# Kernel tuning notes

Hardware: AMD Instinct MI355X
Metric: run time of the kernel (lower is better)

Reference implementation:

```python
import jax, jax.numpy as jnp
import numpy as np
import math

D = 512      # input_size == hidden_size
TAU = 4      # length of att/spatial lists
N = 16384    # tokens (batch*H*W)

def setup_inputs() -> dict:
    key = jax.random.key(0)
    ks = jax.random.split(key, 16)
    s = 1.0 / math.sqrt(D)
    return {
        "T_t": jax.random.normal(ks[0], (N, D), jnp.float32),
        "S_t": jax.random.normal(ks[1], (N, D), jnp.float32),
        "t_att": jax.random.normal(ks[2], (TAU, N, D), jnp.float32),
        "s_att": jax.random.normal(ks[3], (TAU, N, D), jnp.float32),
        "t_spatial": jax.random.normal(ks[4], (TAU, N, D), jnp.float32),
        "s_spatial": jax.random.normal(ks[5], (TAU, N, D), jnp.float32),
        # fl_t: Linear(D, 3D); fl_t_next: Linear(D, D); same for s
        "W_t": jax.random.uniform(ks[6], (3 * D, D), jnp.float32, -s, s),
        "b_t": jax.random.uniform(ks[7], (3 * D,), jnp.float32, -s, s),
        "W_tn": jax.random.uniform(ks[8], (D, D), jnp.float32, -s, s),
        "b_tn": jax.random.uniform(ks[9], (D,), jnp.float32, -s, s),
        "W_s": jax.random.uniform(ks[10], (3 * D, D), jnp.float32, -s, s),
        "b_s": jax.random.uniform(ks[11], (3 * D,), jnp.float32, -s, s),
        "W_sn": jax.random.uniform(ks[12], (D, D), jnp.float32, -s, s),
        "b_sn": jax.random.uniform(ks[13], (D,), jnp.float32, -s, s),
    }

def reference(T_t, S_t, t_att, s_att, t_spatial, s_spatial,
              W_t, b_t, W_tn, b_tn, W_s, b_s, W_sn, b_sn):
    d = T_t.shape[-1]
    scale = 1.0 / jnp.sqrt(jnp.asarray(d, T_t.dtype))
    s_next = S_t @ W_sn.T + b_sn          # [N, D]
    t_next = T_t @ W_tn.T + b_tn          # [N, D]

    # trend weights: dot-product along feature dim, softmax over tau axis
    w_s = jax.nn.softmax(jnp.einsum('knd,nd->kn', s_att, s_next) * scale, axis=0)
    w_t = jax.nn.softmax(jnp.einsum('knd,nd->kn', t_spatial, t_next) * scale, axis=0)
    T_trend = jnp.einsum('knd,kn->nd', t_att, w_s)      # [N, D]
    S_trend = jnp.einsum('knd,kn->nd', s_spatial, w_t)  # [N, D]

    t_gate = jax.nn.sigmoid(t_next)
    s_gate = jax.nn.sigmoid(s_next)
    T_fusion = T_t * t_gate + (1.0 - t_gate) * T_trend
    S_fusion = S_t * s_gate + (1.0 - s_gate) * S_trend

    T_concat = T_fusion @ W_t.T + b_t     # [N, 3D]
    S_concat = S_fusion @ W_s.T + b_s
    t_g, t_t, t_s = jnp.split(T_concat, 3, axis=1)
    s_g, s_t, s_s = jnp.split(S_concat, 3, axis=1)
    T_gate = jax.nn.sigmoid(t_g)
    S_gate = jax.nn.sigmoid(s_g)
    T_new = T_gate * t_t + (1.0 - T_gate) * s_t
    S_new = S_gate * s_s + (1.0 - S_gate) * t_s
    return T_new, S_new
```

## Files before the change

### kernel.cpp

```cpp
#include <hip/hip_runtime.h>

#define NTOK 16384
#define DIM 512
#define NTAU 4

typedef __attribute__((ext_vector_type(4))) float f32x4;
typedef __attribute__((ext_vector_type(8))) short bf16x8;
typedef __attribute__((ext_vector_type(4))) unsigned short u16x4;
typedef __attribute__((ext_vector_type(8))) unsigned short u16x8;
typedef unsigned int u32;

__device__ inline unsigned short f2bf(float f) {
    union { float f; unsigned int u; } v; v.f = f;
    unsigned int u = v.u + 0x7FFFu + ((v.u >> 16) & 1u);
    return (unsigned short)(u >> 16);
}

__device__ inline void bf8_to_f32(u16x8 h, f32x4& a, f32x4& b) {
    union { unsigned int u; float f; } t;
#pragma unroll
    for (int e = 0; e < 4; e++) { t.u = ((unsigned int)h[e]) << 16; a[e] = t.f; }
#pragma unroll
    for (int e = 0; e < 4; e++) { t.u = ((unsigned int)h[4 + e]) << 16; b[e] = t.f; }
}

#define NTLOAD4(p) __builtin_nontemporal_load((const f32x4*)(p))

__device__ __forceinline__ void gload16(const void* g, void* l) {
    __builtin_amdgcn_global_load_lds((const __attribute__((address_space(1))) u32*)g,
                                     (__attribute__((address_space(3))) u32*)l, 16, 0, 0);
}

__global__ void convert_all(const float* __restrict__ a, const float* __restrict__ b,
                            const float* __restrict__ c, const float* __restrict__ d,
                            unsigned short* __restrict__ oa, unsigned short* __restrict__ ob,
                            unsigned short* __restrict__ oc, unsigned short* __restrict__ od) {
    int i = blockIdx.x * 256 + threadIdx.x;
    const float* s; unsigned short* t; int off;
    if (i < 65536)       { s = a; t = oa; off = i; }
    else if (i < 131072) { s = b; t = ob; off = i - 65536; }
    else if (i < 327680) { s = c; t = oc; off = i - 131072; }
    else                 { s = d; t = od; off = i - 327680; }
    f32x4 v = ((const f32x4*)s)[off];
    u16x4 o;
    o[0] = f2bf(v[0]); o[1] = f2bf(v[1]); o[2] = f2bf(v[2]); o[3] = f2bf(v[3]);
    ((u16x4*)t)[off] = o;
}

__global__ __launch_bounds__(256, 2) void gemm_next2(
    const float* __restrict__ T_t, const float* __restrict__ S_t,
    const unsigned short* __restrict__ Wtn, const unsigned short* __restrict__ Wsn,
    const float* __restrict__ btn, const float* __restrict__ bsn,
    unsigned short* __restrict__ t_next, unsigned short* __restrict__ s_next)
{
    __shared__ unsigned short lA[128][40];
    __shared__ unsigned short lB[128][40];
    const int tid = threadIdx.x;
    const int id = blockIdx.x;
    const int xcd = id & 7;
    const int rest = id >> 3;
    const int mat = rest & 1;
    const int idx = rest >> 1;
    const float* A = mat ? S_t : T_t;
    const unsigned short* W = mat ? Wsn : Wtn;
    const float* bias = mat ? bsn : btn;
    unsigned short* out = mat ? s_next : t_next;
    const int m0 = (xcd * 16 + (idx >> 2)) * 128;
    const int n0 = (idx & 3) * 128;
    const int lane = tid & 63;
    const int w = tid >> 6;
    const int wr = w >> 1, wc = w & 1;

    f32x4 acc[4][4];
#pragma unroll
    for (int i = 0; i < 4; i++)
#pragma unroll
        for (int j = 0; j < 4; j++) acc[i][j] = (f32x4){0.f, 0.f, 0.f, 0.f};

    const int arow = tid >> 3;
    const int acol = (tid & 7) * 4;
    const int brow = tid >> 2;
    const int bcol = (tid & 3) * 8;

    for (int k0 = 0; k0 < DIM; k0 += 32) {
#pragma unroll
        for (int i = 0; i < 4; i++) {
            int r = arow + 32 * i;
            f32x4 v = *(const f32x4*)(A + (size_t)(m0 + r) * DIM + k0 + acol);
            u16x4 o;
            o[0] = f2bf(v[0]); o[1] = f2bf(v[1]); o[2] = f2bf(v[2]); o[3] = f2bf(v[3]);
            *(u16x4*)&lA[r][acol] = o;
        }
#pragma unroll
        for (int i = 0; i < 2; i++) {
            int r = brow + 64 * i;
            u16x8 v = *(const u16x8*)(W + (size_t)(n0 + r) * DIM + k0 + bcol);
            *(u16x8*)&lB[r][bcol] = v;
        }
        __syncthreads();

        bf16x8 af[4], bfr[4];
#pragma unroll
        for (int i = 0; i < 4; i++)
            af[i] = *(const bf16x8*)&lA[wr * 64 + i * 16 + (lane & 15)][(lane >> 4) * 8];
#pragma unroll
        for (int j = 0; j < 4; j++)
            bfr[j] = *(const bf16x8*)&lB[wc * 64 + j * 16 + (lane & 15)][(lane >> 4) * 8];
#pragma unroll
        for (int i = 0; i < 4; i++)
#pragma unroll
            for (int j = 0; j < 4; j++)
                acc[i][j] = __builtin_amdgcn_mfma_f32_16x16x32_bf16(af[i], bfr[j], acc[i][j], 0, 0, 0);
        __syncthreads();
    }

#pragma unroll
    for (int j = 0; j < 4; j++) {
        int n = n0 + wc * 64 + j * 16 + (lane & 15);
        float bv = bias[n];
#pragma unroll
        for (int i = 0; i < 4; i++) {
            int mbase = m0 + wr * 64 + i * 16 + (lane >> 4) * 4;
#pragma unroll
            for (int r = 0; r < 4; r++)
                out[(size_t)(mbase + r) * DIM + n] = f2bf(acc[i][j][r] + bv);
        }
    }
}

__global__ __launch_bounds__(256) void dots_kernel(
    const float* __restrict__ s_att, const float* __restrict__ t_spatial,
    const unsigned short* __restrict__ t_next, const unsigned short* __restrict__ s_next,
    float* __restrict__ w_all)
{
    const int lane = threadIdx.x & 63;
    const int id = blockIdx.x;
    const int n = (id & 7) * 2048 + (id >> 3) * 4 + (threadIdx.x >> 6);
    const int c = lane * 8;
    const size_t rb = (size_t)n * DIM + c;
    const float scale = 0.04419417382415922f;

    f32x4 tn_a, tn_b, sn_a, sn_b;
    bf8_to_f32(*(const u16x8*)(t_next + rb), tn_a, tn_b);
    bf8_to_f32(*(const u16x8*)(s_next + rb), sn_a, sn_b);

    float dws[NTAU], dwt[NTAU];
#pragma unroll
    for (int k = 0; k < NTAU; k++) {
        const size_t kb = ((size_t)k * NTOK + n) * DIM + c;
        f32x4 a0 = NTLOAD4(s_att + kb);
        f32x4 a1 = NTLOAD4(s_att + kb + 4);
        f32x4 b0 = NTLOAD4(t_spatial + kb);
        f32x4 b1 = NTLOAD4(t_spatial + kb + 4);
        dws[k] = a0[0]*sn_a[0]+a0[1]*sn_a[1]+a0[2]*sn_a[2]+a0[3]*sn_a[3]
               + a1[0]*sn_b[0]+a1[1]*sn_b[1]+a1[2]*sn_b[2]+a1[3]*sn_b[3];
        dwt[k] = b0[0]*tn_a[0]+b0[1]*tn_a[1]+b0[2]*tn_a[2]+b0[3]*tn_a[3]
               + b1[0]*tn_b[0]+b1[1]*tn_b[1]+b1[2]*tn_b[2]+b1[3]*tn_b[3];
    }
#pragma unroll
    for (int k = 0; k < NTAU; k++) {
        float v = dws[k];
#pragma unroll
        for (int off = 32; off; off >>= 1) v += __shfl_xor(v, off);
        dws[k] = v * scale;
        float u = dwt[k];
#pragma unroll
        for (int off = 32; off; off >>= 1) u += __shfl_xor(u, off);
        dwt[k] = u * scale;
    }

    float ms = fmaxf(fmaxf(dws[0], dws[1]), fmaxf(dws[2], dws[3]));
    float mt = fmaxf(fmaxf(dwt[0], dwt[1]), fmaxf(dwt[2], dwt[3]));
    f32x4 wsv, wtv;
    float ssum = 0.f, tsum = 0.f;
#pragma unroll
    for (int k = 0; k < NTAU; k++) {
        wsv[k] = __expf(dws[k] - ms); ssum += wsv[k];
        wtv[k] = __expf(dwt[k] - mt); tsum += wtv[k];
    }
    float rs = 1.f / ssum, rt = 1.f / tsum;
#pragma unroll
    for (int k = 0; k < NTAU; k++) { wsv[k] *= rs; wtv[k] *= rt; }

    if (lane == 0) {
        *(f32x4*)(w_all + (size_t)n * 8)     = wsv;
        *(f32x4*)(w_all + (size_t)n * 8 + 4) = wtv;
    }
}

__global__ __launch_bounds__(256) void fusion_kernel(
    const float* __restrict__ T_t, const float* __restrict__ S_t,
    const float* __restrict__ t_att, const float* __restrict__ s_spatial,
    const unsigned short* __restrict__ t_next, const unsigned short* __restrict__ s_next,
    const float* __restrict__ w_all,
    unsigned short* __restrict__ Tf, unsigned short* __restrict__ Sf)
{
    const int lane = threadIdx.x & 63;
    const int id = blockIdx.x;
    const int n = (id & 7) * 2048 + (id >> 3) * 4 + (threadIdx.x >> 6);
    const int c = lane * 8;
    const size_t rb = (size_t)n * DIM + c;

    f32x4 wsv = *(const f32x4*)(w_all + (size_t)n * 8);
    f32x4 wtv = *(const f32x4*)(w_all + (size_t)n * 8 + 4);

    f32x4 Tta = {0,0,0,0}, Ttb = {0,0,0,0}, Sta = {0,0,0,0}, Stb = {0,0,0,0};
#pragma unroll
    for (int k = 0; k < NTAU; k++) {
        const size_t kb = ((size_t)k * NTOK + n) * DIM + c;
        f32x4 ta = NTLOAD4(t_att + kb);
        f32x4 tb = NTLOAD4(t_att + kb + 4);
        f32x4 sa = NTLOAD4(s_spatial + kb);
        f32x4 sb = NTLOAD4(s_spatial + kb + 4);
        float wk = wsv[k], vk = wtv[k];
#pragma unroll
        for (int e = 0; e < 4; e++) {
            Tta[e] += wk * ta[e]; Ttb[e] += wk * tb[e];
            Sta[e] += vk * sa[e]; Stb[e] += vk * sb[e];
        }
    }

    f32x4 tn_a, tn_b, sn_a, sn_b;
    bf8_to_f32(*(const u16x8*)(t_next + rb), tn_a, tn_b);
    bf8_to_f32(*(const u16x8*)(s_next + rb), sn_a, sn_b);
    f32x4 Ta = NTLOAD4(T_t + rb);
    f32x4 Tb = NTLOAD4(T_t + rb + 4);
    f32x4 Sa = NTLOAD4(S_t + rb);
    f32x4 Sb = NTLOAD4(S_t + rb + 4);

    u16x8 oT, oS;
#pragma unroll
    for (int e = 0; e < 4; e++) {
        float gt_a = 1.f / (1.f + __expf(-tn_a[e]));
        float gt_b = 1.f / (1.f + __expf(-tn_b[e]));
        float gs_a = 1.f / (1.f + __expf(-sn_a[e]));
        float gs_b = 1.f / (1.f + __expf(-sn_b[e]));
        oT[e]     = f2bf(Ta[e] * gt_a + (1.f - gt_a) * Tta[e]);
        oT[4 + e] = f2bf(Tb[e] * gt_b + (1.f - gt_b) * Ttb[e]);
        oS[e]     = f2bf(Sa[e] * gs_a + (1.f - gs_a) * Sta[e]);
        oS[4 + e] = f2bf(Sb[e] * gs_b + (1.f - gs_b) * Stb[e]);
    }
    *(u16x8*)(Tf + rb) = oT;
    *(u16x8*)(Sf + rb) = oS;
}

__global__ __launch_bounds__(512, 2) void gemm_final(
    const unsigned short* __restrict__ Tf, const unsigned short* __restrict__ Sf,
    const unsigned short* __restrict__ Wt, const unsigned short* __restrict__ Ws,
    const float* __restrict__ bt, const float* __restrict__ bs,
    float* __restrict__ out)
{
    __shared__ __align__(16) unsigned char smem[57344];
    const int tid = threadIdx.x;
    const int id = blockIdx.x;
    const int xcd = id & 7;
    const int idx = id >> 3;
    const int m0 = (xcd * 16 + (idx >> 4)) * 128;
    const int j0 = (idx & 15) * 32;
    const int lane = tid & 63;
    const int w = tid >> 6;
    const int side = w >> 2;
    const int mh = (w >> 1) & 1;
    const int jq = w & 1;

    f32x4 acc[3][4];
#pragma unroll
    for (int g = 0; g < 3; g++)
#pragma unroll
        for (int i = 0; i < 4; i++) acc[g][i] = (f32x4){0.f, 0.f, 0.f, 0.f};

    const int srow = lane >> 2;
    const int sg   = lane & 3;

    const unsigned short* gp[4];
    int nvalid[4];
#pragma unroll
    for (int i = 0; i < 4; i++) {
        const int ch = i * 8 + w;
        nvalid[i] = (ch < 28);
        const unsigned short* p = Tf;
        if (ch < 8) {
            const int trow = ch * 16 + srow;
            const int lg = sg ^ ((trow >> 1) & 3);
            p = Tf + (size_t)(m0 + trow) * DIM + lg * 8;
        } else if (ch < 16) {
            const int trow = (ch - 8) * 16 + srow;
            const int lg = sg ^ ((trow >> 1) & 3);
            p = Sf + (size_t)(m0 + trow) * DIM + lg * 8;
        } else if (ch < 28) {
            const int r = (ch - 16) * 16 + srow;
            const int lg = sg ^ ((r >> 1) & 3);
            const int g = r >> 5;
            const unsigned short* src = (g < 3) ? Wt : Ws;
            const int wrow = (g < 3 ? g : g - 3) * DIM + j0 + (r & 31);
            p = src + (size_t)wrow * DIM + lg * 8;
        }
        gp[i] = p;
    }

    int axo[4], bwo[3];
#pragma unroll
    for (int i = 0; i < 4; i++) {
        const int row = mh * 64 + i * 16 + (lane & 15);
        const int pg = (lane >> 4) ^ ((row >> 1) & 3);
        axo[i] = ((side * 128 + row) * 32 + pg * 8) * 2;
    }
#pragma unroll
    for (int g = 0; g < 3; g++) {
        const int r = (side * 3 + g) * 32 + jq * 16 + (lane & 15);
        const int pg = (lane >> 4) ^ ((r >> 1) & 3);
        bwo[g] = ((256 + r) * 32 + pg * 8) * 2;
    }

    auto stage = [&](int buf) {
#pragma unroll
        for (int i = 0; i < 4; i++) {
            if (nvalid[i])
                gload16(gp[i], smem + buf * 28672 + (i * 8 + w) * 1024);
        }
    };

    stage(0);
    __syncthreads();

    int cur = 0;
    for (int kt = 0; kt < 16; ++kt) {
        if (kt < 15) {
#pragma unroll
            for (int i = 0; i < 4; i++) gp[i] += 32;
            stage(cur ^ 1);
        }

        const unsigned char* base = smem + cur * 28672;
        bf16x8 ax[4], bw[3];
#pragma unroll
        for (int i = 0; i < 4; i++) ax[i] = *(const bf16x8*)(base + axo[i]);
#pragma unroll
        for (int g = 0; g < 3; g++) bw[g] = *(const bf16x8*)(base + bwo[g]);
#pragma unroll
        for (int g = 0; g < 3; g++)
#pragma unroll
            for (int i = 0; i < 4; i++)
                acc[g][i] = __builtin_amdgcn_mfma_f32_16x16x32_bf16(ax[i], bw[g], acc[g][i], 0, 0, 0);

        __syncthreads();
        cur ^= 1;
    }

    const int j = j0 + jq * 16 + (lane & 15);
    const float b0 = side ? bs[j]        : bt[j];
    const float b1 = side ? bs[512 + j]  : bt[512 + j];
    const float b2 = side ? bs[1024 + j] : bt[1024 + j];

    float* exbase = (float*)smem;
    const int col = lane & 15;
#pragma unroll
    for (int i = 0; i < 4; i++) {
        const int rowb = i * 16 + (lane >> 4) * 4;
        f32x4 v = side ? acc[1][i] : acc[2][i];
        const float bb = side ? b1 : b2;
        v[0] += bb; v[1] += bb; v[2] += bb; v[3] += bb;
        *(f32x4*)(exbase + ((w * 16 + col) * 68) + rowb) = v;
    }
    __syncthreads();

    float* obase = out + (side ? (size_t)NTOK * DIM : 0);
    const float bown = side ? b2 : b1;
    const int pw = w ^ 4;
#pragma unroll
    for (int i = 0; i < 4; i++) {
        const int rowb = i * 16 + (lane >> 4) * 4;
        f32x4 oth = *(const f32x4*)(exbase + ((pw * 16 + col) * 68) + rowb);
        f32x4 own = side ? acc[2][i] : acc[1][i];
#pragma unroll
        for (int r = 0; r < 4; r++) {
            const float gate = 1.f / (1.f + __expf(-(acc[0][i][r] + b0)));
            const float ov = own[r] + bown;
            obase[(size_t)(m0 + mh * 64 + rowb + r) * DIM + j] = gate * ov + (1.f - gate) * oth[r];
        }
    }
}

extern "C" void kernel_launch(void* const* d_in, const int* in_sizes, int n_in,
                              void* d_out, int out_size, void* d_ws, size_t ws_size,
                              hipStream_t stream) {
    const float* T_t       = (const float*)d_in[0];
    const float* S_t       = (const float*)d_in[1];
    const float* t_att     = (const float*)d_in[2];
    const float* s_att     = (const float*)d_in[3];
    const float* t_spatial = (const float*)d_in[4];
    const float* s_spatial = (const float*)d_in[5];
    const float* W_t  = (const float*)d_in[6];
    const float* b_t  = (const float*)d_in[7];
    const float* W_tn = (const float*)d_in[8];
    const float* b_tn = (const float*)d_in[9];
    const float* W_s  = (const float*)d_in[10];
    const float* b_s  = (const float*)d_in[11];
    const float* W_sn = (const float*)d_in[12];
    const float* b_sn = (const float*)d_in[13];
    float* out = (float*)d_out;

    char* ws = (char*)d_ws;
    unsigned short* t_next = (unsigned short*)(ws + 0);
    unsigned short* s_next = (unsigned short*)(ws + 16777216);
    unsigned short* Tf     = (unsigned short*)(ws + 33554432);
    unsigned short* Sf     = (unsigned short*)(ws + 50331648);
    unsigned short* Wtn_b  = (unsigned short*)(ws + 67108864);
    unsigned short* Wsn_b  = (unsigned short*)(ws + 67633152);
    unsigned short* Wt_b   = (unsigned short*)(ws + 68157440);
    unsigned short* Ws_b   = (unsigned short*)(ws + 69730304);
    float*          w_all  = (float*)(ws + 71303168);

    convert_all<<<2048, 256, 0, stream>>>(W_tn, W_sn, W_t, W_s,
                                          Wtn_b, Wsn_b, Wt_b, Ws_b);

    gemm_next2<<<1024, 256, 0, stream>>>(T_t, S_t, Wtn_b, Wsn_b, b_tn, b_sn,
                                         t_next, s_next);

    dots_kernel<<<4096, 256, 0, stream>>>(s_att, t_spatial, t_next, s_next, w_all);

    fusion_kernel<<<4096, 256, 0, stream>>>(T_t, S_t, t_att, s_spatial,
                                            t_next, s_next, w_all, Tf, Sf);

    gemm_final<<<2048, 512, 0, stream>>>(Tf, Sf, Wt_b, Ws_b, b_t, b_s, out);
}
```

Baseline: 280.0 us.

## Load weight operands directly into registers in final GEMM, shrink LDS staging

The final fused GEMM no longer stages the weight tiles through shared memory. Each lane now loads its B-fragments straight from global memory into registers, double-buffered one k-step ahead, and only the activation tiles go through LDS, which cuts LDS use from 56KB to 32KB. The exchange buffer layout in the epilogue is also simplified to a per-lane contiguous pattern. The aim is fewer LDS writes and reads and possibly higher occupancy, at the cost of uncoalesced direct global loads of the weights and more register pressure.

```diff
diff --git a/kernel.cpp b/kernel.cpp
--- a/kernel.cpp
+++ b/kernel.cpp
@@ -250,7 +250,7 @@
     const float* __restrict__ bt, const float* __restrict__ bs,
     float* __restrict__ out)
 {
-    __shared__ __align__(16) unsigned char smem[57344];
+    __shared__ __align__(16) unsigned char smem[32768];
     const int tid = threadIdx.x;
     const int id = blockIdx.x;
     const int xcd = id & 7;
@@ -272,111 +272,100 @@
     const int srow = lane >> 2;
     const int sg   = lane & 3;
 
-    const unsigned short* gp[4];
-    int nvalid[4];
-#pragma unroll
-    for (int i = 0; i < 4; i++) {
-        const int ch = i * 8 + w;
-        nvalid[i] = (ch < 28);
-        const unsigned short* p = Tf;
-        if (ch < 8) {
-            const int trow = ch * 16 + srow;
-            const int lg = sg ^ ((trow >> 1) & 3);
-            p = Tf + (size_t)(m0 + trow) * DIM + lg * 8;
-        } else if (ch < 16) {
-            const int trow = (ch - 8) * 16 + srow;
-            const int lg = sg ^ ((trow >> 1) & 3);
-            p = Sf + (size_t)(m0 + trow) * DIM + lg * 8;
-        } else if (ch < 28) {
-            const int r = (ch - 16) * 16 + srow;
-            const int lg = sg ^ ((r >> 1) & 3);
-            const int g = r >> 5;
-            const unsigned short* src = (g < 3) ? Wt : Ws;
-            const int wrow = (g < 3 ? g : g - 3) * DIM + j0 + (r & 31);
-            p = src + (size_t)wrow * DIM + lg * 8;
-        }
-        gp[i] = p;
-    }
-
-    int axo[4], bwo[3];
+    const unsigned short* gsrc[2];
+    int dsto[2];
+#pragma unroll
+    for (int i = 0; i < 2; i++) {
+        const int ch = w * 2 + i;
+        const unsigned short* base = (ch < 8) ? Tf : Sf;
+        const int row = (ch & 7) * 16 + srow;
+        const int lg = sg ^ ((row >> 1) & 3);
+        gsrc[i] = base + (size_t)(m0 + row) * DIM + lg * 8;
+        dsto[i] = ch * 1024;
+    }
+
+    int axo[4];
 #pragma unroll
     for (int i = 0; i < 4; i++) {
         const int row = mh * 64 + i * 16 + (lane & 15);
         const int pg = (lane >> 4) ^ ((row >> 1) & 3);
-        axo[i] = ((side * 128 + row) * 32 + pg * 8) * 2;
-    }
-#pragma unroll
-    for (int g = 0; g < 3; g++) {
-        const int r = (side * 3 + g) * 32 + jq * 16 + (lane & 15);
-        const int pg = (lane >> 4) ^ ((r >> 1) & 3);
-        bwo[g] = ((256 + r) * 32 + pg * 8) * 2;
-    }
-
-    auto stage = [&](int buf) {
-#pragma unroll
-        for (int i = 0; i < 4; i++) {
-            if (nvalid[i])
-                gload16(gp[i], smem + buf * 28672 + (i * 8 + w) * 1024);
-        }
+        axo[i] = side * 8192 + row * 64 + pg * 16;
+    }
+
+    const unsigned short* Wm = side ? Ws : Wt;
+    const int jcol = j0 + jq * 16 + (lane & 15);
+    const unsigned short* bp[3];
+#pragma unroll
+    for (int g = 0; g < 3; g++)
+        bp[g] = Wm + (size_t)(g * 512 + jcol) * DIM + (lane >> 4) * 8;
+
+    auto stageA = [&](int buf) {
+#pragma unroll
+        for (int i = 0; i < 2; i++)
+            gload16(gsrc[i], smem + buf * 16384 + dsto[i]);
     };
 
-    stage(0);
+    bf16x8 bcur[3], bnxt[3];
+    stageA(0);
+#pragma unroll
+    for (int g = 0; g < 3; g++) bcur[g] = *(const bf16x8*)(bp[g]);
+#pragma unroll
+    for (int i = 0; i < 2; i++) gsrc[i] += 32;
+#pragma unroll
+    for (int g = 0; g < 3; g++) bp[g] += 32;
     __syncthreads();
 
     int cur = 0;
     for (int kt = 0; kt < 16; ++kt) {
         if (kt < 15) {
-#pragma unroll
-            for (int i = 0; i < 4; i++) gp[i] += 32;
-            stage(cur ^ 1);
-        }
-
-        const unsigned char* base = smem + cur * 28672;
-        bf16x8 ax[4], bw[3];
-#pragma unroll
-        for (int i = 0; i < 4; i++) ax[i] = *(const bf16x8*)(base + axo[i]);
-#pragma unroll
-        for (int g = 0; g < 3; g++) bw[g] = *(const bf16x8*)(base + bwo[g]);
+            stageA(cur ^ 1);
+#pragma unroll
+            for (int g = 0; g < 3; g++) bnxt[g] = *(const bf16x8*)(bp[g]);
+#pragma unroll
+            for (int i = 0; i < 2; i++) gsrc[i] += 32;
+#pragma unroll
+            for (int g = 0; g < 3; g++) bp[g] += 32;
+        }
+
+        const unsigned char* abase = smem + cur * 16384;
+        bf16x8 ax[4];
+#pragma unroll
+        for (int i = 0; i < 4; i++) ax[i] = *(const bf16x8*)(abase + axo[i]);
 #pragma unroll
         for (int g = 0; g < 3; g++)
 #pragma unroll
             for (int i = 0; i < 4; i++)
-                acc[g][i] = __builtin_amdgcn_mfma_f32_16x16x32_bf16(ax[i], bw[g], acc[g][i], 0, 0, 0);
+                acc[g][i] = __builtin_amdgcn_mfma_f32_16x16x32_bf16(ax[i], bcur[g], acc[g][i], 0, 0, 0);
 
         __syncthreads();
+#pragma unroll
+        for (int g = 0; g < 3; g++) bcur[g] = bnxt[g];
         cur ^= 1;
     }
 
-    const int j = j0 + jq * 16 + (lane & 15);
-    const float b0 = side ? bs[j]        : bt[j];
-    const float b1 = side ? bs[512 + j]  : bt[512 + j];
-    const float b2 = side ? bs[1024 + j] : bt[1024 + j];
-
-    float* exbase = (float*)smem;
-    const int col = lane & 15;
+    const float* bb = side ? bs : bt;
+    const float bg   = bb[jcol];
+    const float bown = side ? bb[1024 + jcol] : bb[512 + jcol];
+    const float bex  = side ? bb[512 + jcol]  : bb[1024 + jcol];
+    float* exf = (float*)smem;
 #pragma unroll
     for (int i = 0; i < 4; i++) {
-        const int rowb = i * 16 + (lane >> 4) * 4;
         f32x4 v = side ? acc[1][i] : acc[2][i];
-        const float bb = side ? b1 : b2;
-        v[0] += bb; v[1] += bb; v[2] += bb; v[3] += bb;
-        *(f32x4*)(exbase + ((w * 16 + col) * 68) + rowb) = v;
+        v[0] += bex; v[1] += bex; v[2] += bex; v[3] += bex;
+        *(f32x4*)(exf + ((w * 4 + i) * 64 + lane) * 4) = v;
     }
     __syncthreads();
 
     float* obase = out + (side ? (size_t)NTOK * DIM : 0);
-    const float bown = side ? b2 : b1;
-    const int pw = w ^ 4;
 #pragma unroll
     for (int i = 0; i < 4; i++) {
-        const int rowb = i * 16 + (lane >> 4) * 4;
-        f32x4 oth = *(const f32x4*)(exbase + ((pw * 16 + col) * 68) + rowb);
+        f32x4 oth = *(const f32x4*)(exf + (((w ^ 4) * 4 + i) * 64 + lane) * 4);
         f32x4 own = side ? acc[2][i] : acc[1][i];
 #pragma unroll
         for (int r = 0; r < 4; r++) {
-            const float gate = 1.f / (1.f + __expf(-(acc[0][i][r] + b0)));
-            const float ov = own[r] + bown;
-            obase[(size_t)(m0 + mh * 64 + rowb + r) * DIM + j] = gate * ov + (1.f - gate) * oth[r];
+            const float gate = 1.f / (1.f + __expf(-(acc[0][i][r] + bg)));
+            obase[(size_t)(m0 + mh * 64 + i * 16 + (lane >> 4) * 4 + r) * DIM + jcol]
+                = gate * (own[r] + bown) + (1.f - gate) * oth[r];
         }
     }
 }
```

After: 321.5 us. 14.8% more time.
